# Performance work log

Measured on AMD Instinct MI355X. Metric: run time of the kernel, lower is better.

Reference implementation:

```python
import jax, jax.numpy as jnp
import numpy as np

NUM_EMB = 8192
DIM = 64
DECAY = 0.99
EPS = 1e-05
COMMIT = 0.25


def setup_inputs() -> dict:
    key = jax.random.key(0)
    k1, k2, k3 = jax.random.split(key, 3)
    inputs = jax.random.normal(k1, (8, 4096, DIM), jnp.float32)
    weight = jax.random.normal(k2, (NUM_EMB, DIM), jnp.float32)
    ema_cluster_count = jnp.ones((NUM_EMB,), jnp.float32)
    ema_weight_sum = jax.random.normal(k3, (NUM_EMB, DIM), jnp.float32)
    return {
        'inputs': inputs,
        'weight': weight,
        'ema_cluster_count': ema_cluster_count,
        'ema_weight_sum': ema_weight_sum,
    }


def reference(inputs, weight, ema_cluster_count, ema_weight_sum):
    flat = inputs.reshape(-1, DIM)  # [N, D]
    distances = (
        jnp.sum(flat ** 2, axis=1, keepdims=True)
        + jnp.sum(weight ** 2, axis=1)
        - 2.0 * flat @ weight.T
    )
    idx = jnp.argmin(distances, axis=1)  # [N] int

    # EMA stats (training branch): one-hot column sums == segment counts,
    # encodings.T @ flat == segment sums of inputs by code index.
    counts = jax.ops.segment_sum(
        jnp.ones(flat.shape[0], jnp.float32), idx, num_segments=NUM_EMB)
    new_cc = ema_cluster_count * DECAY + (1.0 - DECAY) * counts
    emb_sum = jax.ops.segment_sum(flat, idx, num_segments=NUM_EMB)
    new_ws = ema_weight_sum * DECAY + (1.0 - DECAY) * emb_sum

    n = jnp.sum(new_cc)
    smoothed = (new_cc + EPS) / (n + NUM_EMB * EPS) * n
    new_weight = new_ws / smoothed[:, None]  # updated codebook [K, D]

    quantized_raw = new_weight[idx].reshape(inputs.shape)
    e_latent_loss = jnp.mean((jax.lax.stop_gradient(quantized_raw) - inputs) ** 2)
    vq_loss = COMMIT * e_latent_loss

    avg_probs = counts / flat.shape[0]
    perplexity = jnp.exp(-jnp.sum(avg_probs * jnp.log(avg_probs + 1e-10)))

    # straight-through estimator
    quantized = inputs + jax.lax.stop_gradient(quantized_raw - inputs)
    return quantized, vq_loss, idx, perplexity, new_weight, new_cc, new_ws
```

## Files before the change

### kernel.cpp

```cpp
#include <hip/hip_runtime.h>
#include <math.h>

typedef _Float16 f16x8 __attribute__((ext_vector_type(8)));
typedef float f32x4 __attribute__((ext_vector_type(4)));

#define NROWS 32768
#define KEMB  8192

#define DECAYF 0.99f
#define OMDF   0.01f

#define OUT_Q    0
#define OUT_LOSS 2097152
#define OUT_IDX  2097153
#define OUT_PERP 2129921
#define OUT_NW   2129922
#define OUT_NCC  2654210
#define OUT_NWS  2662402

#define WS_N      0
#define WS_ENT    1
#define WS_COUNTS 4
#define WS_EMB    8196
#define WS_IDX    532484
#define WS_W2H    565252
#define WS_WFRAG  573444
#define WS_ZERO_UNITS 532484

__device__ __forceinline__ float sq_rn(float v) { return __fmul_rn(v, v); }

__device__ __forceinline__ float npsumsq64(const float* vbuf) {
  float a[8];
#pragma unroll
  for (int j = 0; j < 8; ++j) a[j] = sq_rn(vbuf[j]);
#pragma unroll
  for (int m = 1; m < 8; ++m)
#pragma unroll
    for (int j = 0; j < 8; ++j) a[j] = __fadd_rn(a[j], sq_rn(vbuf[m*8 + j]));
  return __fadd_rn(__fadd_rn(__fadd_rn(a[0],a[1]), __fadd_rn(a[2],a[3])),
                   __fadd_rn(__fadd_rn(a[4],a[5]), __fadd_rn(a[6],a[7])));
}

__device__ __forceinline__ void split_f16(float x, _Float16& hi, _Float16& lo) {
  hi = (_Float16)x;
  float r = __fsub_rn(x, (float)hi);
  lo = (_Float16)r;
}

__global__ __launch_bounds__(256) void prep_kernel(const float* __restrict__ wg,
                                                   float* __restrict__ ws) {
  const int tid = blockIdx.x * 256 + threadIdx.x;
  if (tid < KEMB) {
    const float* src = wg + (size_t)tid * 64;
    float vbuf[64];
#pragma unroll
    for (int f = 0; f < 16; ++f) {
      float4 v = *(const float4*)(src + f*4);
      vbuf[f*4+0]=v.x; vbuf[f*4+1]=v.y; vbuf[f*4+2]=v.z; vbuf[f*4+3]=v.w;
    }
    ws[WS_W2H + tid] = __fmul_rn(0.5f, npsumsq64(vbuf));
  } else if (tid < KEMB + 65536) {
    const int u = tid - KEMB;
    const int K = u >> 3, g = u & 7;
    const int n = K & 15, P = K >> 4;
    const int slot = (g&3)*16 + n, shi = g >> 2;
    const float* src = wg + (size_t)K*64 + g*8;
    float4 v0 = *(const float4*)src, v1 = *(const float4*)(src + 4);
    float vv[8] = {v0.x,v0.y,v0.z,v0.w,v1.x,v1.y,v1.z,v1.w};
    f16x8 hi, lo;
#pragma unroll
    for (int j = 0; j < 8; ++j) { _Float16 h, l; split_f16(vv[j], h, l); hi[j]=h; lo[j]=l; }
    _Float16* wf = (_Float16*)(ws + WS_WFRAG);
    *(f16x8*)&wf[((size_t)(P*4 + shi)*64 + slot)*8]     = hi;
    *(f16x8*)&wf[((size_t)(P*4 + 2 + shi)*64 + slot)*8] = lo;
  }
}

#define MFMA_CLUSTER(ACC, H0, H1, L0, L1, CW)                                                 \
  __builtin_amdgcn_s_setprio(1);                                                              \
  _Pragma("unroll")                                                                           \
  for (int bt = 0; bt < 4; ++bt) ACC[bt] = __builtin_amdgcn_mfma_f32_16x16x32_f16(H0, b[bt][0], CW,      0,0,0); \
  _Pragma("unroll")                                                                           \
  for (int bt = 0; bt < 4; ++bt) ACC[bt] = __builtin_amdgcn_mfma_f32_16x16x32_f16(H1, b[bt][1], ACC[bt], 0,0,0); \
  _Pragma("unroll")                                                                           \
  for (int bt = 0; bt < 4; ++bt) ACC[bt] = __builtin_amdgcn_mfma_f32_16x16x32_f16(H0, b[bt][2], ACC[bt], 0,0,0); \
  _Pragma("unroll")                                                                           \
  for (int bt = 0; bt < 4; ++bt) ACC[bt] = __builtin_amdgcn_mfma_f32_16x16x32_f16(H1, b[bt][3], ACC[bt], 0,0,0); \
  _Pragma("unroll")                                                                           \
  for (int bt = 0; bt < 4; ++bt) ACC[bt] = __builtin_amdgcn_mfma_f32_16x16x32_f16(L0, b[bt][0], ACC[bt], 0,0,0); \
  _Pragma("unroll")                                                                           \
  for (int bt = 0; bt < 4; ++bt) ACC[bt] = __builtin_amdgcn_mfma_f32_16x16x32_f16(L1, b[bt][1], ACC[bt], 0,0,0); \
  __builtin_amdgcn_s_setprio(0);

#define LOADP(H0, H1, L0, L1, CW, WP, CP)           \
  H0 = *(const f16x8*)(WP);                         \
  H1 = *(const f16x8*)(WP + 512);                   \
  L0 = *(const f16x8*)(WP + 1024);                  \
  L1 = *(const f16x8*)(WP + 1536);                  \
  CW = *(const f32x4*)(CP);                         \
  WP += 16384; CP += 128;

#define TOURN(ACC, C0)                                                       \
  _Pragma("unroll")                                                          \
  for (int bt = 0; bt < 4; ++bt) {                                           \
    const float d0 = ACC[bt][0], d1 = ACC[bt][1], d2 = ACC[bt][2], d3 = ACC[bt][3]; \
    const float m01 = fminf(d0, d1), m23 = fminf(d2, d3);                    \
    const float pm  = fminf(m01, m23);                                       \
    const int i01 = (d1 < d0) ? 1 : 0;                                       \
    const int i23 = (d3 < d2) ? 3 : 2;                                       \
    const int isel = (m23 < m01) ? i23 : i01;                                \
    if (pm < bestd[bt]) { bestd[bt] = pm; bestk[bt] = (C0) + isel; }         \
  }

__global__ __launch_bounds__(256, 2) void argmin_kernel(const float* __restrict__ xg,
                                                        float* __restrict__ out,
                                                        float* __restrict__ ws) {
  __shared__ __align__(16) _Float16 xp[4*4*64*8];
  __shared__ float md[64*4];
  __shared__ int   mk[64*4];
  __shared__ int   bkL[64];

  const int t    = threadIdx.x;
  const int lane = t & 63, wv = t >> 6;
  const int quad = lane >> 4, n16 = lane & 15;
  const int cg = wv;
  const int row0 = blockIdx.x * 64;
  const _Float16* __restrict__ wfrag = (const _Float16*)(ws + WS_WFRAG);
  const float* __restrict__ w2hg = ws + WS_W2H;

#pragma unroll
  for (int it = 0; it < 2; ++it) {
    const int u  = t + 256*it;
    const int rp = u >> 7, n = (u >> 3) & 15, g = u & 7;
    const float* src = xg + (size_t)(row0 + rp*16 + n)*64 + g*8;
    float4 v0 = *(const float4*)src, v1 = *(const float4*)(src + 4);
    float vv[8] = {v0.x,v0.y,v0.z,v0.w,v1.x,v1.y,v1.z,v1.w};
    f16x8 hi, lo;
#pragma unroll
    for (int j = 0; j < 8; ++j) { _Float16 h, l; split_f16(-vv[j], h, l); hi[j]=h; lo[j]=l; }
    const int slot = (g&3)*16 + n, shi = g >> 2;
    *(f16x8*)&xp[(((rp*4) + shi)*64 + slot)*8]     = hi;
    *(f16x8*)&xp[(((rp*4) + 2 + shi)*64 + slot)*8] = lo;
  }
  __syncthreads();

  f16x8 b[4][4];
#pragma unroll
  for (int bt = 0; bt < 4; ++bt)
#pragma unroll
    for (int s = 0; s < 4; ++s)
      b[bt][s] = *(const f16x8*)&xp[(((bt*4) + s)*64 + lane)*8];

  {
    const unsigned ph = (blockIdx.x * 2654435761u) >> 30;
    if (ph & 1) __builtin_amdgcn_s_sleep(2);
    if (ph & 2) __builtin_amdgcn_s_sleep(4);
  }

  float bestd[4]; int bestk[4];
#pragma unroll
  for (int i = 0; i < 4; ++i) { bestd[i] = INFINITY; bestk[i] = 0; }

  const int q4 = quad * 4;

  const _Float16* wpA = wfrag + (size_t)cg * 2048 + (size_t)lane * 8;
  const _Float16* wpB = wpA + 8192;
  const float*    cpA = w2hg + cg*16 + q4;
  const float*    cpB = cpA + 64;

  f16x8 hA0, hA1, lA0, lA1, hB0, hB1, lB0, lB1;
  f32x4 cwA, cwB;

  LOADP(hA0, hA1, lA0, lA1, cwA, wpA, cpA);
  LOADP(hB0, hB1, lB0, lB1, cwB, wpB, cpB);

  f32x4 accA[4], accB[4];
  int c0A = cg*16 + q4;
  int c0B = c0A + 64;

  MFMA_CLUSTER(accA, hA0, hA1, lA0, lA1, cwA);
  LOADP(hA0, hA1, lA0, lA1, cwA, wpA, cpA);

#pragma unroll 1
  for (int j = 0; j < 63; ++j) {
    MFMA_CLUSTER(accB, hB0, hB1, lB0, lB1, cwB);
    LOADP(hB0, hB1, lB0, lB1, cwB, wpB, cpB);
    TOURN(accA, c0A);
    MFMA_CLUSTER(accA, hA0, hA1, lA0, lA1, cwA);
    c0A += 128;
    if (j < 62) { LOADP(hA0, hA1, lA0, lA1, cwA, wpA, cpA); }
    TOURN(accB, c0B);
    c0B += 128;
  }
  MFMA_CLUSTER(accB, hB0, hB1, lB0, lB1, cwB);
  TOURN(accA, c0A);
  TOURN(accB, c0B);

#pragma unroll
  for (int bt = 0; bt < 4; ++bt) {
    float bd = bestd[bt]; int bk = bestk[bt];
#pragma unroll
    for (int m = 16; m < 64; m <<= 1) {
      const float od = __shfl_xor(bd, m, 64);
      const int   ok = __shfl_xor(bk, m, 64);
      if (od < bd || (od == bd && ok < bk)) { bd = od; bk = ok; }
    }
    if (lane < 16) {
      const int row = bt*16 + n16;
      md[row*4 + cg] = bd;
      mk[row*4 + cg] = bk;
    }
  }
  __syncthreads();

  if (t < 64) {
    const int row = t;
    float bd = md[row*4]; int bk = mk[row*4];
#pragma unroll
    for (int u2 = 1; u2 < 4; ++u2) {
      const float d2 = md[row*4 + u2]; const int k2 = mk[row*4 + u2];
      if (d2 < bd || (d2 == bd && k2 < bk)) { bd = d2; bk = k2; }
    }
    out[OUT_IDX + row0 + row] = (float)bk;
    ((int*)ws)[WS_IDX + row0 + row] = bk;
    bkL[row] = bk;
    atomicAdd(&ws[WS_COUNTS + bk], 1.0f);
  }
  __syncthreads();

#pragma unroll 4
  for (int r = 0; r < 16; ++r) {
    const int row = wv*16 + r;
    const int k = bkL[row];
    atomicAdd(&ws[WS_EMB + (size_t)k*64 + lane],
              xg[(size_t)(row0 + row)*64 + lane]);
  }
}

__global__ __launch_bounds__(256) void stats_kernel(const float* __restrict__ cc,
                                                    float* __restrict__ out,
                                                    float* __restrict__ ws) {
  const int t = threadIdx.x;
  float v1 = 0.0f, v2 = 0.0f;
#pragma unroll
  for (int i = 0; i < 32; ++i) {
    const int k = i*256 + t;
    const float cnt = ws[WS_COUNTS + k];
    const float ncc = __fadd_rn(__fmul_rn(DECAYF, cc[k]), __fmul_rn(OMDF, cnt));
    out[OUT_NCC + k] = ncc;
    const float p = cnt * (1.0f/32768.0f);
    v1 += ncc;
    v2 += __fmul_rn(p, logf(__fadd_rn(p, 1e-10f)));
  }
#pragma unroll
  for (int off = 32; off > 0; off >>= 1) {
    v1 += __shfl_down(v1, off);
    v2 += __shfl_down(v2, off);
  }
  __shared__ float s1[4], s2[4];
  const int lane = t & 63, wid = t >> 6;
  if (lane == 0) { s1[wid] = v1; s2[wid] = v2; }
  __syncthreads();
  if (t == 0) {
    ws[WS_N]   = (s1[0]+s1[1]) + (s1[2]+s1[3]);
    ws[WS_ENT] = (s2[0]+s2[1]) + (s2[2]+s2[3]);
  }
}

__global__ __launch_bounds__(256) void update_quant_kernel(const float* __restrict__ xg,
                                                           const float* __restrict__ ws0,
                                                           float* __restrict__ out,
                                                           float* __restrict__ ws) {
  const int t = threadIdx.x;
  const float n = ws[WS_N];
  const float den = __fadd_rn(n, 0.08192f);

  const int e4 = blockIdx.x * 256 + t;
  {
    const int k = e4 >> 4;
    const float ncc = out[OUT_NCC + k];
    const float smoothed = __fmul_rn(__fadd_rn(ncc, 1e-5f) / den, n);
    float4 w0 = *(const float4*)(ws0 + (size_t)e4*4);
    float4 em = *(const float4*)(ws + WS_EMB + (size_t)e4*4);
    float wv4[4] = {w0.x, w0.y, w0.z, w0.w};
    float ev4[4] = {em.x, em.y, em.z, em.w};
    float nwsv[4], nwv[4];
#pragma unroll
    for (int i = 0; i < 4; ++i) {
      nwsv[i] = __fadd_rn(__fmul_rn(DECAYF, wv4[i]), __fmul_rn(OMDF, ev4[i]));
      nwv[i]  = nwsv[i] / smoothed;
    }
    float4 onws = {nwsv[0], nwsv[1], nwsv[2], nwsv[3]};
    float4 onw  = {nwv[0],  nwv[1],  nwv[2],  nwv[3]};
    *(float4*)(out + OUT_NWS + (size_t)e4*4) = onws;
    *(float4*)(out + OUT_NW  + (size_t)e4*4) = onw;
    if (e4 == 0) out[OUT_PERP] = expf(-ws[WS_ENT]);
  }

  const int* idxb = (const int*)ws + WS_IDX;
  float v = 0.0f;
#pragma unroll
  for (int j = 0; j < 4; ++j) {
    const int qe4 = (j*512 + blockIdx.x)*256 + t;
    const int row = qe4 >> 4, d = (qe4 & 15) * 4;
    const int k = idxb[row];
    const float ncc = out[OUT_NCC + k];
    const float smK = __fmul_rn(__fadd_rn(ncc, 1e-5f) / den, n);
    float4 wq = *(const float4*)(ws0 + (size_t)k*64 + d);
    float4 eq = *(const float4*)(ws + WS_EMB + (size_t)k*64 + d);
    float4 x  = *(const float4*)(xg + (size_t)qe4*4);
    float wv4[4] = {wq.x,wq.y,wq.z,wq.w};
    float ev4[4] = {eq.x,eq.y,eq.z,eq.w};
    float xv[4]  = {x.x,x.y,x.z,x.w};
    float4 o; float ov[4];
#pragma unroll
    for (int i = 0; i < 4; ++i) {
      const float nws = __fadd_rn(__fmul_rn(DECAYF, wv4[i]), __fmul_rn(OMDF, ev4[i]));
      const float q = nws / smK;
      const float df = __fsub_rn(q, xv[i]);
      ov[i] = __fadd_rn(xv[i], df);
      v = fmaf(df, df, v);
    }
    o.x = ov[0]; o.y = ov[1]; o.z = ov[2]; o.w = ov[3];
    *(float4*)(out + OUT_Q + (size_t)qe4*4) = o;
  }
#pragma unroll
  for (int off = 32; off > 0; off >>= 1) v += __shfl_down(v, off);
  __shared__ float sm[4];
  const int lane = t & 63, wid = t >> 6;
  if (lane == 0) sm[wid] = v;
  __syncthreads();
  if (t == 0) ws[WS_COUNTS + blockIdx.x] = (sm[0]+sm[1]) + (sm[2]+sm[3]);
}

__global__ void final_kernel(float* __restrict__ out, const float* __restrict__ ws) {
  const int t = threadIdx.x;
  float v = 0.0f;
#pragma unroll
  for (int i = 0; i < 8; ++i) v += ws[WS_COUNTS + i*64 + t];
#pragma unroll
  for (int off = 32; off > 0; off >>= 1) v += __shfl_down(v, off);
  if (t == 0) out[OUT_LOSS] = __fmul_rn(0.25f, v / 2097152.0f);
}

extern "C" void kernel_launch(void* const* d_in, const int* in_sizes, int n_in,
                              void* d_out, int out_size, void* d_ws, size_t ws_size,
                              hipStream_t stream) {
  (void)in_sizes; (void)n_in; (void)out_size; (void)ws_size;
  const float* x   = (const float*)d_in[0];
  const float* w   = (const float*)d_in[1];
  const float* cc  = (const float*)d_in[2];
  const float* ws0 = (const float*)d_in[3];
  float* out = (float*)d_out;
  float* ws  = (float*)d_ws;

  hipMemsetAsync(d_ws, 0, (size_t)WS_ZERO_UNITS * 4, stream);
  hipLaunchKernelGGL(prep_kernel,         dim3(288), dim3(256), 0, stream, w, ws);
  hipLaunchKernelGGL(argmin_kernel,       dim3(512), dim3(256), 0, stream, x, out, ws);
  hipLaunchKernelGGL(stats_kernel,        dim3(1),   dim3(256), 0, stream, cc, out, ws);
  hipLaunchKernelGGL(update_quant_kernel, dim3(512), dim3(256), 0, stream, x, ws0, out, ws);
  hipLaunchKernelGGL(final_kernel,        dim3(1),   dim3(64),  0, stream, out, ws);
}
```

Before: 177.8 us.

## Process four codebook panels per iteration instead of A/B double-buffered pairs

Replaces the two-way A/B ping-pong MFMA pipeline with a loop that loads four codebook panels at once and issues 96 MFMAs per iteration across 16 accumulators, then runs the argmin tournament on all four. It also removes the per-block staggered s_sleep start. The aim is more independent MFMA work per load, giving more latency hiding and fewer loop iterations. The cost is higher register pressure (64 accumulator floats plus four fragment sets), and loads are no longer overlapped with the tournament of the previous panel, which may hurt occupancy at launch bounds of 2.

```diff
diff --git a/kernel.cpp b/kernel.cpp
--- a/kernel.cpp
+++ b/kernel.cpp
@@ -76,30 +76,6 @@
   }
 }
 
-#define MFMA_CLUSTER(ACC, H0, H1, L0, L1, CW)                                                 \
-  __builtin_amdgcn_s_setprio(1);                                                              \
-  _Pragma("unroll")                                                                           \
-  for (int bt = 0; bt < 4; ++bt) ACC[bt] = __builtin_amdgcn_mfma_f32_16x16x32_f16(H0, b[bt][0], CW,      0,0,0); \
-  _Pragma("unroll")                                                                           \
-  for (int bt = 0; bt < 4; ++bt) ACC[bt] = __builtin_amdgcn_mfma_f32_16x16x32_f16(H1, b[bt][1], ACC[bt], 0,0,0); \
-  _Pragma("unroll")                                                                           \
-  for (int bt = 0; bt < 4; ++bt) ACC[bt] = __builtin_amdgcn_mfma_f32_16x16x32_f16(H0, b[bt][2], ACC[bt], 0,0,0); \
-  _Pragma("unroll")                                                                           \
-  for (int bt = 0; bt < 4; ++bt) ACC[bt] = __builtin_amdgcn_mfma_f32_16x16x32_f16(H1, b[bt][3], ACC[bt], 0,0,0); \
-  _Pragma("unroll")                                                                           \
-  for (int bt = 0; bt < 4; ++bt) ACC[bt] = __builtin_amdgcn_mfma_f32_16x16x32_f16(L0, b[bt][0], ACC[bt], 0,0,0); \
-  _Pragma("unroll")                                                                           \
-  for (int bt = 0; bt < 4; ++bt) ACC[bt] = __builtin_amdgcn_mfma_f32_16x16x32_f16(L1, b[bt][1], ACC[bt], 0,0,0); \
-  __builtin_amdgcn_s_setprio(0);
-
-#define LOADP(H0, H1, L0, L1, CW, WP, CP)           \
-  H0 = *(const f16x8*)(WP);                         \
-  H1 = *(const f16x8*)(WP + 512);                   \
-  L0 = *(const f16x8*)(WP + 1024);                  \
-  L1 = *(const f16x8*)(WP + 1536);                  \
-  CW = *(const f32x4*)(CP);                         \
-  WP += 16384; CP += 128;
-
 #define TOURN(ACC, C0)                                                       \
   _Pragma("unroll")                                                          \
   for (int bt = 0; bt < 4; ++bt) {                                           \
@@ -151,50 +127,81 @@
     for (int s = 0; s < 4; ++s)
       b[bt][s] = *(const f16x8*)&xp[(((bt*4) + s)*64 + lane)*8];
 
-  {
-    const unsigned ph = (blockIdx.x * 2654435761u) >> 30;
-    if (ph & 1) __builtin_amdgcn_s_sleep(2);
-    if (ph & 2) __builtin_amdgcn_s_sleep(4);
-  }
-
   float bestd[4]; int bestk[4];
 #pragma unroll
   for (int i = 0; i < 4; ++i) { bestd[i] = INFINITY; bestk[i] = 0; }
 
   const int q4 = quad * 4;
 
-  const _Float16* wpA = wfrag + (size_t)cg * 2048 + (size_t)lane * 8;
-  const _Float16* wpB = wpA + 8192;
-  const float*    cpA = w2hg + cg*16 + q4;
-  const float*    cpB = cpA + 64;
-
-  f16x8 hA0, hA1, lA0, lA1, hB0, hB1, lB0, lB1;
-  f32x4 cwA, cwB;
-
-  LOADP(hA0, hA1, lA0, lA1, cwA, wpA, cpA);
-  LOADP(hB0, hB1, lB0, lB1, cwB, wpB, cpB);
-
-  f32x4 accA[4], accB[4];
-  int c0A = cg*16 + q4;
-  int c0B = c0A + 64;
-
-  MFMA_CLUSTER(accA, hA0, hA1, lA0, lA1, cwA);
-  LOADP(hA0, hA1, lA0, lA1, cwA, wpA, cpA);
+  const _Float16* wp[4];
+  const float*    cp[4];
+#pragma unroll
+  for (int P = 0; P < 4; ++P) {
+    wp[P] = wfrag + (size_t)(cg + 4*P) * 2048 + (size_t)lane * 8;
+    cp[P] = w2hg + (cg + 4*P)*16 + q4;
+  }
+
+  f16x8 sh0[4], sh1[4], sl0[4], sl1[4];
+  f32x4 scw[4];
+
+#define LOADSET(P)                                   \
+  sh0[P] = *(const f16x8*)(wp[P]);                   \
+  sh1[P] = *(const f16x8*)(wp[P] + 512);             \
+  sl0[P] = *(const f16x8*)(wp[P] + 1024);            \
+  sl1[P] = *(const f16x8*)(wp[P] + 1536);            \
+  scw[P] = *(const f32x4*)(cp[P]);                   \
+  wp[P] += 32768; cp[P] += 256;
+
+#pragma unroll
+  for (int P = 0; P < 4; ++P) { LOADSET(P) }
+
+  f32x4 acc[4][4];
+  int cbase = cg*16 + q4;
 
 #pragma unroll 1
-  for (int j = 0; j < 63; ++j) {
-    MFMA_CLUSTER(accB, hB0, hB1, lB0, lB1, cwB);
-    LOADP(hB0, hB1, lB0, lB1, cwB, wpB, cpB);
-    TOURN(accA, c0A);
-    MFMA_CLUSTER(accA, hA0, hA1, lA0, lA1, cwA);
-    c0A += 128;
-    if (j < 62) { LOADP(hA0, hA1, lA0, lA1, cwA, wpA, cpA); }
-    TOURN(accB, c0B);
-    c0B += 128;
-  }
-  MFMA_CLUSTER(accB, hB0, hB1, lB0, lB1, cwB);
-  TOURN(accA, c0A);
-  TOURN(accB, c0B);
+  for (int m = 0; m < 32; ++m) {
+    __builtin_amdgcn_s_setprio(1);
+#pragma unroll
+    for (int P = 0; P < 4; ++P)
+#pragma unroll
+      for (int bt = 0; bt < 4; ++bt)
+        acc[P][bt] = __builtin_amdgcn_mfma_f32_16x16x32_f16(sh0[P], b[bt][0], scw[P], 0,0,0);
+#pragma unroll
+    for (int P = 0; P < 4; ++P)
+#pragma unroll
+      for (int bt = 0; bt < 4; ++bt)
+        acc[P][bt] = __builtin_amdgcn_mfma_f32_16x16x32_f16(sh1[P], b[bt][1], acc[P][bt], 0,0,0);
+#pragma unroll
+    for (int P = 0; P < 4; ++P)
+#pragma unroll
+      for (int bt = 0; bt < 4; ++bt)
+        acc[P][bt] = __builtin_amdgcn_mfma_f32_16x16x32_f16(sh0[P], b[bt][2], acc[P][bt], 0,0,0);
+#pragma unroll
+    for (int P = 0; P < 4; ++P)
+#pragma unroll
+      for (int bt = 0; bt < 4; ++bt)
+        acc[P][bt] = __builtin_amdgcn_mfma_f32_16x16x32_f16(sh1[P], b[bt][3], acc[P][bt], 0,0,0);
+#pragma unroll
+    for (int P = 0; P < 4; ++P)
+#pragma unroll
+      for (int bt = 0; bt < 4; ++bt)
+        acc[P][bt] = __builtin_amdgcn_mfma_f32_16x16x32_f16(sl0[P], b[bt][0], acc[P][bt], 0,0,0);
+#pragma unroll
+    for (int P = 0; P < 4; ++P)
+#pragma unroll
+      for (int bt = 0; bt < 4; ++bt)
+        acc[P][bt] = __builtin_amdgcn_mfma_f32_16x16x32_f16(sl1[P], b[bt][1], acc[P][bt], 0,0,0);
+    __builtin_amdgcn_s_setprio(0);
+
+    if (m < 31) {
+#pragma unroll
+      for (int P = 0; P < 4; ++P) { LOADSET(P) }
+    }
+
+#pragma unroll
+    for (int P = 0; P < 4; ++P) { TOURN(acc[P], cbase + 64*P) }
+    cbase += 256;
+  }
 
 #pragma unroll
   for (int bt = 0; bt < 4; ++bt) {
```

Result: slower. 204.1 us (+14.8%).

## Interleave A/B MFMA chains in one loop body and drop staggered sleep

Applied to the files above, without the earlier changes.

Replaces the software-pipelined loop, which alternated an MFMA cluster for one codebook tile with the tournament of the other, with a loop that interleaves the A and B MFMA chains instruction by instruction. Both tiles' fragment loads are then issued after the MFMAs, followed by both tournaments. The per-block s_sleep stagger is removed, and launch bounds are expressed as amdgpu waves_per_eu(2,2). The goal is to hide MFMA dependency latency with two independent chains. In exchange, loads are no longer overlapped with the previous tile's MFMAs, so memory latency may be exposed.

```diff
diff --git a/kernel.cpp b/kernel.cpp
--- a/kernel.cpp
+++ b/kernel.cpp
@@ -76,22 +76,6 @@
   }
 }
 
-#define MFMA_CLUSTER(ACC, H0, H1, L0, L1, CW)                                                 \
-  __builtin_amdgcn_s_setprio(1);                                                              \
-  _Pragma("unroll")                                                                           \
-  for (int bt = 0; bt < 4; ++bt) ACC[bt] = __builtin_amdgcn_mfma_f32_16x16x32_f16(H0, b[bt][0], CW,      0,0,0); \
-  _Pragma("unroll")                                                                           \
-  for (int bt = 0; bt < 4; ++bt) ACC[bt] = __builtin_amdgcn_mfma_f32_16x16x32_f16(H1, b[bt][1], ACC[bt], 0,0,0); \
-  _Pragma("unroll")                                                                           \
-  for (int bt = 0; bt < 4; ++bt) ACC[bt] = __builtin_amdgcn_mfma_f32_16x16x32_f16(H0, b[bt][2], ACC[bt], 0,0,0); \
-  _Pragma("unroll")                                                                           \
-  for (int bt = 0; bt < 4; ++bt) ACC[bt] = __builtin_amdgcn_mfma_f32_16x16x32_f16(H1, b[bt][3], ACC[bt], 0,0,0); \
-  _Pragma("unroll")                                                                           \
-  for (int bt = 0; bt < 4; ++bt) ACC[bt] = __builtin_amdgcn_mfma_f32_16x16x32_f16(L0, b[bt][0], ACC[bt], 0,0,0); \
-  _Pragma("unroll")                                                                           \
-  for (int bt = 0; bt < 4; ++bt) ACC[bt] = __builtin_amdgcn_mfma_f32_16x16x32_f16(L1, b[bt][1], ACC[bt], 0,0,0); \
-  __builtin_amdgcn_s_setprio(0);
-
 #define LOADP(H0, H1, L0, L1, CW, WP, CP)           \
   H0 = *(const f16x8*)(WP);                         \
   H1 = *(const f16x8*)(WP + 512);                   \
@@ -112,9 +96,10 @@
     if (pm < bestd[bt]) { bestd[bt] = pm; bestk[bt] = (C0) + isel; }         \
   }
 
-__global__ __launch_bounds__(256, 2) void argmin_kernel(const float* __restrict__ xg,
-                                                        float* __restrict__ out,
-                                                        float* __restrict__ ws) {
+__global__ __attribute__((amdgpu_flat_work_group_size(256,256), amdgpu_waves_per_eu(2,2)))
+void argmin_kernel(const float* __restrict__ xg,
+                   float* __restrict__ out,
+                   float* __restrict__ ws) {
   __shared__ __align__(16) _Float16 xp[4*4*64*8];
   __shared__ float md[64*4];
   __shared__ int   mk[64*4];
@@ -151,12 +136,6 @@
     for (int s = 0; s < 4; ++s)
       b[bt][s] = *(const f16x8*)&xp[(((bt*4) + s)*64 + lane)*8];
 
-  {
-    const unsigned ph = (blockIdx.x * 2654435761u) >> 30;
-    if (ph & 1) __builtin_amdgcn_s_sleep(2);
-    if (ph & 2) __builtin_amdgcn_s_sleep(4);
-  }
-
   float bestd[4]; int bestk[4];
 #pragma unroll
   for (int i = 0; i < 4; ++i) { bestd[i] = INFINITY; bestk[i] = 0; }
@@ -178,23 +157,45 @@
   int c0A = cg*16 + q4;
   int c0B = c0A + 64;
 
-  MFMA_CLUSTER(accA, hA0, hA1, lA0, lA1, cwA);
-  LOADP(hA0, hA1, lA0, lA1, cwA, wpA, cpA);
-
 #pragma unroll 1
-  for (int j = 0; j < 63; ++j) {
-    MFMA_CLUSTER(accB, hB0, hB1, lB0, lB1, cwB);
-    LOADP(hB0, hB1, lB0, lB1, cwB, wpB, cpB);
+  for (int j = 0; j < 64; ++j) {
+    __builtin_amdgcn_s_setprio(1);
+#pragma unroll
+    for (int bt = 0; bt < 4; ++bt) accA[bt] = __builtin_amdgcn_mfma_f32_16x16x32_f16(hA0, b[bt][0], cwA,      0,0,0);
+#pragma unroll
+    for (int bt = 0; bt < 4; ++bt) accB[bt] = __builtin_amdgcn_mfma_f32_16x16x32_f16(hB0, b[bt][0], cwB,      0,0,0);
+#pragma unroll
+    for (int bt = 0; bt < 4; ++bt) accA[bt] = __builtin_amdgcn_mfma_f32_16x16x32_f16(hA1, b[bt][1], accA[bt], 0,0,0);
+#pragma unroll
+    for (int bt = 0; bt < 4; ++bt) accB[bt] = __builtin_amdgcn_mfma_f32_16x16x32_f16(hB1, b[bt][1], accB[bt], 0,0,0);
+#pragma unroll
+    for (int bt = 0; bt < 4; ++bt) accA[bt] = __builtin_amdgcn_mfma_f32_16x16x32_f16(hA0, b[bt][2], accA[bt], 0,0,0);
+#pragma unroll
+    for (int bt = 0; bt < 4; ++bt) accB[bt] = __builtin_amdgcn_mfma_f32_16x16x32_f16(hB0, b[bt][2], accB[bt], 0,0,0);
+#pragma unroll
+    for (int bt = 0; bt < 4; ++bt) accA[bt] = __builtin_amdgcn_mfma_f32_16x16x32_f16(hA1, b[bt][3], accA[bt], 0,0,0);
+#pragma unroll
+    for (int bt = 0; bt < 4; ++bt) accB[bt] = __builtin_amdgcn_mfma_f32_16x16x32_f16(hB1, b[bt][3], accB[bt], 0,0,0);
+#pragma unroll
+    for (int bt = 0; bt < 4; ++bt) accA[bt] = __builtin_amdgcn_mfma_f32_16x16x32_f16(lA0, b[bt][0], accA[bt], 0,0,0);
+#pragma unroll
+    for (int bt = 0; bt < 4; ++bt) accB[bt] = __builtin_amdgcn_mfma_f32_16x16x32_f16(lB0, b[bt][0], accB[bt], 0,0,0);
+#pragma unroll
+    for (int bt = 0; bt < 4; ++bt) accA[bt] = __builtin_amdgcn_mfma_f32_16x16x32_f16(lA1, b[bt][1], accA[bt], 0,0,0);
+#pragma unroll
+    for (int bt = 0; bt < 4; ++bt) accB[bt] = __builtin_amdgcn_mfma_f32_16x16x32_f16(lB1, b[bt][1], accB[bt], 0,0,0);
+    __builtin_amdgcn_s_setprio(0);
+
+    if (j < 63) {
+      LOADP(hA0, hA1, lA0, lA1, cwA, wpA, cpA);
+      LOADP(hB0, hB1, lB0, lB1, cwB, wpB, cpB);
+    }
+
     TOURN(accA, c0A);
-    MFMA_CLUSTER(accA, hA0, hA1, lA0, lA1, cwA);
     c0A += 128;
-    if (j < 62) { LOADP(hA0, hA1, lA0, lA1, cwA, wpA, cpA); }
     TOURN(accB, c0B);
     c0B += 128;
   }
-  MFMA_CLUSTER(accB, hB0, hB1, lB0, lB1, cwB);
-  TOURN(accA, c0A);
-  TOURN(accB, c0B);
 
 #pragma unroll
   for (int bt = 0; bt < 4; ++bt) {
```

After: 178.5 us. No clear change (+0.4%).
